# Kernel tuning notes

Hardware: AMD Instinct MI355X
Metric: run time of the kernel (lower is better)

Reference implementation:

```python
import jax, jax.numpy as jnp
import numpy as np

# DeformConv1d config (matches init_kwargs)
K = 3          # kernel_size
DIL = 1        # dilation
STRIDE = 1
PAD = DIL * (K - 1)  # 'same' total padding = 2 -> (1,1) reflect


def setup_inputs() -> dict:
    key = jax.random.key(0)
    k1, k2, k3, k4 = jax.random.split(key, 4)
    B, C, L = 16, 64, 8192
    O = 64
    x = jax.random.normal(k1, (B, C, L), dtype=jnp.float32)
    offsets = jax.random.normal(k2, (B, 1, L, K), dtype=jnp.float32)
    weight = jax.random.normal(k3, (O, C, K), dtype=jnp.float32) * (1.0 / np.sqrt(C * K))
    bias = jax.random.normal(k4, (O,), dtype=jnp.float32) * 0.01
    return {"x": x, "offsets": offsets, "weight": weight, "bias": bias}


def _deform_conv1d(x, offsets, weight, bias):
    # reflect 'same' padding: left = PAD//2, right = PAD - PAD//2
    left = PAD // 2
    x_pad = jnp.pad(x, ((0, 0), (0, 0), (left, PAD - left)), mode="reflect")
    B, C, Lp = x_pad.shape
    OL = offsets.shape[-2]
    dt = x.dtype

    dilated = (jnp.arange(K, dtype=dt) * DIL)          # [K] = [0, d, ..., d(K-1)]
    t0 = (jnp.arange(OL, dtype=dt) * STRIDE)[:, None]  # [OL, 1]

    # sampling positions T: [B, G, OL, K], constrained to kernel receptive field
    T = t0 + dilated + offsets
    T = jnp.maximum(T, t0)
    T = jnp.minimum(T, t0 + dilated[-1])

    # integer lower neighbors (no grad through floor); clamp so U+1 is valid
    U = jnp.clip(jnp.floor(T).astype(jnp.int32), 0, Lp - 2)  # [B, G, OL, K]

    # gather both neighbors along length axis (broadcast offset group -> C)
    idx = jnp.broadcast_to(U, (B, C, OL, K)).reshape(B, C, OL * K)
    x0 = jnp.take_along_axis(x_pad, idx, axis=2).reshape(B, C, OL, K)
    x1 = jnp.take_along_axis(x_pad, idx + 1, axis=2).reshape(B, C, OL, K)

    # linear interpolation weights G = max(0, 1 - |U - T|)
    Uf = U.astype(dt)
    w0 = jnp.maximum(0.0, 1.0 - jnp.abs(Uf - T))        # [B, G, OL, K]
    w1 = jnp.maximum(0.0, 1.0 - jnp.abs(Uf + 1.0 - T))
    sampled = w0 * x0 + w1 * x1                          # [B, C, OL, K]

    # conv1d(weight, stride=K) on flattened [B, C, OL*K] == per-position contraction
    out = jnp.einsum("bcok,fck->bfo", sampled, weight) + bias[None, :, None]
    return out


def reference(x, offsets, weight, bias):
    return _deform_conv1d(x, offsets, weight, bias)
```

## Files before the change

### kernel.cpp

```cpp
#include <hip/hip_runtime.h>
#include <stdint.h>

#define BB   16
#define CC   64
#define LL   8192
#define OO   64
#define KK   3
#define TT   64
#define XSW  72
#define SW   200

typedef __attribute__((ext_vector_type(8))) short short8;
typedef __attribute__((ext_vector_type(4))) float float4_t;

__device__ __forceinline__ ushort f2bf(float f) {
    uint32_t u = __float_as_uint(f);
    return (ushort)((u + 0x7FFFu + ((u >> 16) & 1u)) >> 16);
}
__device__ __forceinline__ float bf2f(ushort h) {
    return __uint_as_float(((uint32_t)h) << 16);
}

__global__ __launch_bounds__(256, 4) void deform_main(
    const float* __restrict__ x, const float* __restrict__ offs,
    const float* __restrict__ w, const float* __restrict__ bias,
    float* __restrict__ out) {

    __shared__ ushort buf[TT * SW];
    __shared__ ushort xs[67 * XSW];
    __shared__ int    Ul[TT * KK];
    __shared__ float  W0s[TT * KK], W1s[TT * KK];

    const int tid  = threadIdx.x;
    const int bb   = blockIdx.x >> 7;
    const int tile = blockIdx.x & 127;
    const int ts   = tile * TT;

    {
        const float4_t* src = (const float4_t*)w;
        #pragma unroll
        for (int i = 0; i < 12; i++) {
            int idx4 = tid + i * 256;
            float4_t v = src[idx4];
            int f  = idx4 / 48;
            int e0 = (idx4 - f * 48) * 4;
            #pragma unroll
            for (int j = 0; j < 4; j++) {
                int e = e0 + j;
                int c = e / 3;
                int k = e - c * 3;
                buf[f * SW + k * 64 + c] = f2bf(v[j]);
            }
        }
    }

    {
        const float* xb = x + (size_t)bb * (CC * LL);
        #pragma unroll
        for (int i = 0; i < 17; i++) {
            int idx = tid + i * 256;
            if (idx < 64 * 67) {
                int c = idx / 67;
                int p = idx - c * 67;
                int j = ts + p - 1;
                if (j < 0) j = -j;
                if (j >= LL) j = 2 * LL - 2 - j;
                xs[p * XSW + c] = f2bf(xb[c * LL + j]);
            }
        }
    }

    if (tid < TT * KK) {
        int n = tid / 3;
        int k = tid - n * 3;
        float off = offs[((size_t)bb * LL + ts + n) * 3 + k];
        float t0  = (float)(ts + n);
        float T   = t0 + (float)k + off;
        T = fmaxf(T, t0);
        T = fminf(T, t0 + 2.0f);
        int U = (int)floorf(T);
        if (U > LL) U = LL;
        float Uf = (float)U;
        Ul[tid]  = U - ts;
        W0s[tid] = fmaxf(0.0f, 1.0f - fabsf(Uf - T));
        W1s[tid] = fmaxf(0.0f, 1.0f - fabsf(Uf + 1.0f - T));
    }
    __syncthreads();

    const int lane = tid & 63;
    const int wv   = tid >> 6;
    const int lr   = lane & 15;
    const int q    = lane >> 4;

    short8 a[6];
    #pragma unroll
    for (int kk = 0; kk < 6; kk++)
        a[kk] = *(const short8*)&buf[(wv * 16 + lr) * SW + kk * 32 + q * 8];
    __syncthreads();

    #pragma unroll
    for (int i = 0; i < 6; i++) {
        int tau = tid + i * 256;
        int g   = tau & 7;
        int nk  = tau >> 3;
        int n   = nk / 3;
        int k   = nk - n * 3;
        int u   = Ul[nk];
        float w0 = W0s[nk], w1 = W1s[nk];
        int c0  = g * 8;
        union { uint4 v; ushort u16[8]; } r0, r1;
        r0.v = *(const uint4*)&xs[u * XSW + c0];
        r1.v = *(const uint4*)&xs[(u + 1) * XSW + c0];
        uint32_t pk[4];
        #pragma unroll
        for (int j = 0; j < 4; j++) {
            float v0 = w0 * bf2f(r0.u16[2 * j])     + w1 * bf2f(r1.u16[2 * j]);
            float v1 = w0 * bf2f(r0.u16[2 * j + 1]) + w1 * bf2f(r1.u16[2 * j + 1]);
            pk[j] = (uint32_t)f2bf(v0) | ((uint32_t)f2bf(v1) << 16);
        }
        uint4 ov;
        ov.x = pk[0]; ov.y = pk[1]; ov.z = pk[2]; ov.w = pk[3];
        *(uint4*)&buf[n * SW + k * 64 + c0] = ov;
    }
    __syncthreads();

    float4_t acc0 = {0.f, 0.f, 0.f, 0.f};
    float4_t acc1 = acc0, acc2 = acc0, acc3 = acc0;

    #pragma unroll
    for (int kk = 0; kk < 6; kk++) {
        int k0 = kk * 32 + q * 8;
        short8 b0 = *(const short8*)&buf[( 0 + lr) * SW + k0];
        short8 b1 = *(const short8*)&buf[(16 + lr) * SW + k0];
        short8 b2 = *(const short8*)&buf[(32 + lr) * SW + k0];
        short8 b3 = *(const short8*)&buf[(48 + lr) * SW + k0];
        acc0 = __builtin_amdgcn_mfma_f32_16x16x32_bf16(a[kk], b0, acc0, 0, 0, 0);
        acc1 = __builtin_amdgcn_mfma_f32_16x16x32_bf16(a[kk], b1, acc1, 0, 0, 0);
        acc2 = __builtin_amdgcn_mfma_f32_16x16x32_bf16(a[kk], b2, acc2, 0, 0, 0);
        acc3 = __builtin_amdgcn_mfma_f32_16x16x32_bf16(a[kk], b3, acc3, 0, 0, 0);
    }

    const int f0 = wv * 16 + q * 4;
    float4_t bv = *(const float4_t*)&bias[f0];
    float* ob = out + ((size_t)bb * OO + f0) * LL + ts;
    #pragma unroll
    for (int r = 0; r < 4; r++) {
        float* orow = ob + (size_t)r * LL;
        orow[ 0 + lr] = acc0[r] + bv[r];
        orow[16 + lr] = acc1[r] + bv[r];
        orow[32 + lr] = acc2[r] + bv[r];
        orow[48 + lr] = acc3[r] + bv[r];
    }
}

extern "C" void kernel_launch(void* const* d_in, const int* in_sizes, int n_in,
                              void* d_out, int out_size, void* d_ws, size_t ws_size,
                              hipStream_t stream) {
    (void)d_ws; (void)ws_size;
    const float* x    = (const float*)d_in[0];
    const float* offs = (const float*)d_in[1];
    const float* w    = (const float*)d_in[2];
    const float* bias = (const float*)d_in[3];
    float* out = (float*)d_out;

    hipLaunchKernelGGL(deform_main, dim3(BB * (LL / TT)), dim3(256), 0, stream,
                       x, offs, w, bias, out);
}
```

Baseline: 104.1 us.

## Process two tiles per block with register prefetch of next tile's input

Each block now handles two consecutive 64-position tiles, so the grid is halved and the weight staging is paid once per two tiles. While the current tile is interpolated and run through the MFMAs, the next tile's x slice and offsets are loaded into registers and written to shared memory after the matrix multiply. The reduction axis is reordered from k-major to c-major interleaving, which lets the weight staging and the sampled-value writes use vectorized shared-memory stores. The extra prefetch registers under launch bounds of 4 blocks per CU risk spilling, and fewer blocks means less parallelism to hide latency.

```diff
diff --git a/kernel.cpp b/kernel.cpp
--- a/kernel.cpp
+++ b/kernel.cpp
@@ -7,6 +7,7 @@
 #define OO   64
 #define KK   3
 #define TT   64
+#define NT   2
 #define XSW  72
 #define SW   200
 
@@ -26,64 +27,67 @@
     const float* __restrict__ w, const float* __restrict__ bias,
     float* __restrict__ out) {
 
-    __shared__ ushort buf[TT * SW];
-    __shared__ ushort xs[67 * XSW];
+    __shared__ __attribute__((aligned(16))) ushort buf[TT * SW];
+    __shared__ __attribute__((aligned(16))) ushort xs[67 * XSW];
     __shared__ int    Ul[TT * KK];
     __shared__ float  W0s[TT * KK], W1s[TT * KK];
 
     const int tid  = threadIdx.x;
-    const int bb   = blockIdx.x >> 7;
-    const int tile = blockIdx.x & 127;
-    const int ts   = tile * TT;
-
-    {
-        const float4_t* src = (const float4_t*)w;
-        #pragma unroll
-        for (int i = 0; i < 12; i++) {
-            int idx4 = tid + i * 256;
-            float4_t v = src[idx4];
-            int f  = idx4 / 48;
-            int e0 = (idx4 - f * 48) * 4;
-            #pragma unroll
-            for (int j = 0; j < 4; j++) {
-                int e = e0 + j;
-                int c = e / 3;
-                int k = e - c * 3;
-                buf[f * SW + k * 64 + c] = f2bf(v[j]);
-            }
-        }
-    }
-
-    {
-        const float* xb = x + (size_t)bb * (CC * LL);
-        #pragma unroll
-        for (int i = 0; i < 17; i++) {
-            int idx = tid + i * 256;
-            if (idx < 64 * 67) {
-                int c = idx / 67;
-                int p = idx - c * 67;
-                int j = ts + p - 1;
-                if (j < 0) j = -j;
-                if (j >= LL) j = 2 * LL - 2 - j;
-                xs[p * XSW + c] = f2bf(xb[c * LL + j]);
-            }
-        }
-    }
-
+    const int bb   = blockIdx.x >> 6;
+    const int pair = blockIdx.x & 63;
+    const int ts0  = pair * (TT * NT);
+
+    const float* xb = x + (size_t)bb * (CC * LL);
+
+    float4_t wreg[12];
+    #pragma unroll
+    for (int i = 0; i < 12; i++) wreg[i] = ((const float4_t*)w)[tid + i * 256];
+
+    float xr[17];
+    #pragma unroll
+    for (int i = 0; i < 17; i++) {
+        int idx = tid + i * 256;
+        if (idx < CC * 67) {
+            int c = idx / 67, p = idx - c * 67;
+            int j = ts0 + p - 1;
+            if (j < 0) j = -j;
+            if (j >= LL) j = 2 * LL - 2 - j;
+            xr[i] = xb[c * LL + j];
+        }
+    }
+    float offv = 0.f;
+    if (tid < TT * KK) offv = offs[(size_t)bb * LL * KK + ts0 * KK + tid];
+
+    #pragma unroll
+    for (int i = 0; i < 12; i++) {
+        int idx4 = tid + i * 256;
+        int f  = idx4 / 48;
+        int e0 = (idx4 - f * 48) * 4;
+        uint2 pk;
+        pk.x = (uint32_t)f2bf(wreg[i].x) | ((uint32_t)f2bf(wreg[i].y) << 16);
+        pk.y = (uint32_t)f2bf(wreg[i].z) | ((uint32_t)f2bf(wreg[i].w) << 16);
+        *(uint2*)&buf[f * SW + e0] = pk;
+    }
+    #pragma unroll
+    for (int i = 0; i < 17; i++) {
+        int idx = tid + i * 256;
+        if (idx < CC * 67) {
+            int c = idx / 67, p = idx - c * 67;
+            xs[p * XSW + c] = f2bf(xr[i]);
+        }
+    }
     if (tid < TT * KK) {
-        int n = tid / 3;
-        int k = tid - n * 3;
-        float off = offs[((size_t)bb * LL + ts + n) * 3 + k];
-        float t0  = (float)(ts + n);
-        float T   = t0 + (float)k + off;
-        T = fmaxf(T, t0);
-        T = fminf(T, t0 + 2.0f);
+        int n = tid / 3, k = tid - n * 3;
+        float t0v = (float)(ts0 + n);
+        float T = t0v + (float)k + offv;
+        T = fmaxf(T, t0v);
+        T = fminf(T, t0v + 2.0f);
         int U = (int)floorf(T);
         if (U > LL) U = LL;
         float Uf = (float)U;
-        Ul[tid]  = U - ts;
-        W0s[tid] = fmaxf(0.0f, 1.0f - fabsf(Uf - T));
-        W1s[tid] = fmaxf(0.0f, 1.0f - fabsf(Uf + 1.0f - T));
+        Ul[tid]  = U - ts0;
+        W0s[tid] = fmaxf(0.f, 1.f - fabsf(Uf - T));
+        W1s[tid] = fmaxf(0.f, 1.f - fabsf(Uf + 1.f - T));
     }
     __syncthreads();
 
@@ -99,57 +103,111 @@
     __syncthreads();
 
     #pragma unroll
-    for (int i = 0; i < 6; i++) {
-        int tau = tid + i * 256;
-        int g   = tau & 7;
-        int nk  = tau >> 3;
-        int n   = nk / 3;
-        int k   = nk - n * 3;
-        int u   = Ul[nk];
-        float w0 = W0s[nk], w1 = W1s[nk];
-        int c0  = g * 8;
-        union { uint4 v; ushort u16[8]; } r0, r1;
-        r0.v = *(const uint4*)&xs[u * XSW + c0];
-        r1.v = *(const uint4*)&xs[(u + 1) * XSW + c0];
-        uint32_t pk[4];
+    for (int t = 0; t < NT; t++) {
+        const int ts = ts0 + t * TT;
+
         #pragma unroll
-        for (int j = 0; j < 4; j++) {
-            float v0 = w0 * bf2f(r0.u16[2 * j])     + w1 * bf2f(r1.u16[2 * j]);
-            float v1 = w0 * bf2f(r0.u16[2 * j + 1]) + w1 * bf2f(r1.u16[2 * j + 1]);
-            pk[j] = (uint32_t)f2bf(v0) | ((uint32_t)f2bf(v1) << 16);
-        }
-        uint4 ov;
-        ov.x = pk[0]; ov.y = pk[1]; ov.z = pk[2]; ov.w = pk[3];
-        *(uint4*)&buf[n * SW + k * 64 + c0] = ov;
-    }
-    __syncthreads();
-
-    float4_t acc0 = {0.f, 0.f, 0.f, 0.f};
-    float4_t acc1 = acc0, acc2 = acc0, acc3 = acc0;
-
-    #pragma unroll
-    for (int kk = 0; kk < 6; kk++) {
-        int k0 = kk * 32 + q * 8;
-        short8 b0 = *(const short8*)&buf[( 0 + lr) * SW + k0];
-        short8 b1 = *(const short8*)&buf[(16 + lr) * SW + k0];
-        short8 b2 = *(const short8*)&buf[(32 + lr) * SW + k0];
-        short8 b3 = *(const short8*)&buf[(48 + lr) * SW + k0];
-        acc0 = __builtin_amdgcn_mfma_f32_16x16x32_bf16(a[kk], b0, acc0, 0, 0, 0);
-        acc1 = __builtin_amdgcn_mfma_f32_16x16x32_bf16(a[kk], b1, acc1, 0, 0, 0);
-        acc2 = __builtin_amdgcn_mfma_f32_16x16x32_bf16(a[kk], b2, acc2, 0, 0, 0);
-        acc3 = __builtin_amdgcn_mfma_f32_16x16x32_bf16(a[kk], b3, acc3, 0, 0, 0);
-    }
-
-    const int f0 = wv * 16 + q * 4;
-    float4_t bv = *(const float4_t*)&bias[f0];
-    float* ob = out + ((size_t)bb * OO + f0) * LL + ts;
-    #pragma unroll
-    for (int r = 0; r < 4; r++) {
-        float* orow = ob + (size_t)r * LL;
-        orow[ 0 + lr] = acc0[r] + bv[r];
-        orow[16 + lr] = acc1[r] + bv[r];
-        orow[32 + lr] = acc2[r] + bv[r];
-        orow[48 + lr] = acc3[r] + bv[r];
+        for (int i = 0; i < 2; i++) {
+            int tau = tid + i * 256;
+            int n = tau >> 3, c0 = (tau & 7) * 8;
+            uint32_t wrd[12];
+            #pragma unroll
+            for (int m = 0; m < 12; m++) wrd[m] = 0;
+            #pragma unroll
+            for (int k = 0; k < 3; k++) {
+                int u = Ul[n * 3 + k];
+                float w0 = W0s[n * 3 + k], w1 = W1s[n * 3 + k];
+                union { uint4 v; ushort u16[8]; } r0, r1;
+                r0.v = *(const uint4*)&xs[u * XSW + c0];
+                r1.v = *(const uint4*)&xs[(u + 1) * XSW + c0];
+                #pragma unroll
+                for (int j = 0; j < 8; j++) {
+                    float val = w0 * bf2f(r0.u16[j]) + w1 * bf2f(r1.u16[j]);
+                    int e = j * 3 + k;
+                    wrd[e >> 1] |= (uint32_t)f2bf(val) << ((e & 1) * 16);
+                }
+            }
+            ushort* dst = &buf[n * SW + c0 * 3];
+            #pragma unroll
+            for (int m = 0; m < 3; m++) {
+                uint4 ov;
+                ov.x = wrd[4 * m]; ov.y = wrd[4 * m + 1];
+                ov.z = wrd[4 * m + 2]; ov.w = wrd[4 * m + 3];
+                *(uint4*)&dst[m * 8] = ov;
+            }
+        }
+
+        float xr2[17];
+        float offv2 = 0.f;
+        if (t + 1 < NT) {
+            const int ts1 = ts + TT;
+            #pragma unroll
+            for (int i = 0; i < 17; i++) {
+                int idx = tid + i * 256;
+                if (idx < CC * 67) {
+                    int c = idx / 67, p = idx - c * 67;
+                    int j = ts1 + p - 1;
+                    if (j < 0) j = -j;
+                    if (j >= LL) j = 2 * LL - 2 - j;
+                    xr2[i] = xb[c * LL + j];
+                }
+            }
+            if (tid < TT * KK) offv2 = offs[(size_t)bb * LL * KK + ts1 * KK + tid];
+        }
+        __syncthreads();
+
+        float4_t acc0 = {0.f, 0.f, 0.f, 0.f};
+        float4_t acc1 = acc0, acc2 = acc0, acc3 = acc0;
+        #pragma unroll
+        for (int kk = 0; kk < 6; kk++) {
+            int k0 = kk * 32 + q * 8;
+            short8 b0 = *(const short8*)&buf[( 0 + lr) * SW + k0];
+            short8 b1 = *(const short8*)&buf[(16 + lr) * SW + k0];
+            short8 b2 = *(const short8*)&buf[(32 + lr) * SW + k0];
+            short8 b3 = *(const short8*)&buf[(48 + lr) * SW + k0];
+            acc0 = __builtin_amdgcn_mfma_f32_16x16x32_bf16(a[kk], b0, acc0, 0, 0, 0);
+            acc1 = __builtin_amdgcn_mfma_f32_16x16x32_bf16(a[kk], b1, acc1, 0, 0, 0);
+            acc2 = __builtin_amdgcn_mfma_f32_16x16x32_bf16(a[kk], b2, acc2, 0, 0, 0);
+            acc3 = __builtin_amdgcn_mfma_f32_16x16x32_bf16(a[kk], b3, acc3, 0, 0, 0);
+        }
+
+        if (t + 1 < NT) {
+            const int ts1 = ts + TT;
+            #pragma unroll
+            for (int i = 0; i < 17; i++) {
+                int idx = tid + i * 256;
+                if (idx < CC * 67) {
+                    int c = idx / 67, p = idx - c * 67;
+                    xs[p * XSW + c] = f2bf(xr2[i]);
+                }
+            }
+            if (tid < TT * KK) {
+                int n = tid / 3, k = tid - n * 3;
+                float t0v = (float)(ts1 + n);
+                float T = t0v + (float)k + offv2;
+                T = fmaxf(T, t0v);
+                T = fminf(T, t0v + 2.0f);
+                int U = (int)floorf(T);
+                if (U > LL) U = LL;
+                float Uf = (float)U;
+                Ul[tid]  = U - ts1;
+                W0s[tid] = fmaxf(0.f, 1.f - fabsf(Uf - T));
+                W1s[tid] = fmaxf(0.f, 1.f - fabsf(Uf + 1.f - T));
+            }
+        }
+
+        const int f0 = wv * 16 + q * 4;
+        float4_t bv = *(const float4_t*)&bias[f0];
+        float* ob = out + ((size_t)bb * OO + f0) * LL + ts;
+        #pragma unroll
+        for (int r = 0; r < 4; r++) {
+            float* orow = ob + (size_t)r * LL;
+            orow[ 0 + lr] = acc0[r] + bv[r];
+            orow[16 + lr] = acc1[r] + bv[r];
+            orow[32 + lr] = acc2[r] + bv[r];
+            orow[48 + lr] = acc3[r] + bv[r];
+        }
+        __syncthreads();
     }
 }
 
@@ -163,6 +221,6 @@
     const float* bias = (const float*)d_in[3];
     float* out = (float*)d_out;
 
-    hipLaunchKernelGGL(deform_main, dim3(BB * (LL / TT)), dim3(256), 0, stream,
+    hipLaunchKernelGGL(deform_main, dim3(BB * (LL / (TT * NT))), dim3(256), 0, stream,
                        x, offs, w, bias, out);
 }
```

Result: faster. 99.46 us (-4.4%).
